# Performance work log

Hardware: AMD Instinct MI355X
Metric: run time of the kernel (lower is better)

The kernel has to match this reference:

```python
import jax, jax.numpy as jnp
import numpy as np

EPS = 1e-5

def _silu(x):
    return x * jax.nn.sigmoid(x)

def _layernorm(x, g, b):
    mu = jnp.mean(x, axis=-1, keepdims=True)
    var = jnp.mean((x - mu) ** 2, axis=-1, keepdims=True)
    return (x - mu) * jax.lax.rsqrt(var + EPS) * g + b

def _mamba(x, in_w, conv_w, conv_b, xproj_w, dt_w, dt_b, A_log, Dp, out_w):
    # x: (B, L, dm); faithful mamba-ssm block: in_proj -> causal dwconv -> silu ->
    # x_proj -> softplus(dt_proj) -> selective scan -> gate -> out_proj
    B, L, dm = x.shape
    di, K = conv_w.shape          # d_inner, d_conv
    ds = A_log.shape[1]           # d_state
    dtr = dt_w.shape[1]           # dt_rank
    xz = x @ in_w.T               # (B, L, 2*di)
    xi, z = jnp.split(xz, 2, axis=-1)
    # causal depthwise conv1d (pad K-1 on the left), kernel unrolled (K=4)
    xpad = jnp.pad(xi, ((0, 0), (K - 1, 0), (0, 0)))
    xc = conv_b + sum(conv_w[:, k] * xpad[:, k:k + L, :] for k in range(K))
    xc = _silu(xc)                # (B, L, di)
    xdbl = xc @ xproj_w.T         # (B, L, dtr + 2*ds)
    dt, Bm, Cm = jnp.split(xdbl, [dtr, dtr + ds], axis=-1)
    delta = jax.nn.softplus(dt @ dt_w.T + dt_b)        # (B, L, di)
    A = -jnp.exp(A_log)                                # (di, ds)
    dA = jnp.exp(delta[..., None] * A)                 # (B, L, di, ds)
    dBu = delta[..., None] * Bm[:, :, None, :] * xc[..., None]
    def step(h, inp):
        dA_t, dBu_t, C_t = inp                         # (B,di,ds),(B,di,ds),(B,ds)
        h = dA_t * h + dBu_t
        y = jnp.einsum('bdn,bn->bd', h, C_t)
        return h, y
    h0 = jnp.zeros((B, di, ds), dtype=x.dtype)
    _, ys = jax.lax.scan(step, h0, (dA.transpose(1, 0, 2, 3),
                                    dBu.transpose(1, 0, 2, 3),
                                    Cm.transpose(1, 0, 2)))
    y = ys.transpose(1, 0, 2) + xc * Dp                # (B, L, di)
    y = y * _silu(z)
    return y @ out_w.T                                 # (B, L, dm)

def _forward(t1, t2, t3, t4, t5,
             m0_in_w, m0_conv_w, m0_conv_b, m0_xproj_w, m0_dt_w, m0_dt_b, m0_Alog, m0_D, m0_out_w,
             m1_in_w, m1_conv_w, m1_conv_b, m1_xproj_w, m1_dt_w, m1_dt_b, m1_Alog, m1_D, m1_out_w,
             norm_g, norm_b, proj_w, proj_b, norm1_g, norm1_b, proj1_w, proj1_b, skip_scale):
    B = t1.shape[0]
    flat = lambda t, c: t.reshape(B, c, -1).transpose(0, 2, 1)   # (B, N, C)
    f1, f2, f3, f4, f5 = flat(t1, 8), flat(t2, 16), flat(t3, 24), flat(t4, 32), flat(t5, 48)
    c1 = jnp.concatenate([f1[:, :, 0:8], f2[:, :, 0:8], f3[:, :, 0:8], f4[:, :, 0:8], f5[:, :, 0:8]], axis=1)   # (B,21824,8)
    c2 = jnp.concatenate([f2[:, :, 8:16], f3[:, :, 8:16], f4[:, :, 8:16], f5[:, :, 8:16]], axis=1)              # (B,5440,8)
    c3 = jnp.concatenate([f3[:, :, 16:24], f4[:, :, 16:24], f5[:, :, 16:24]], axis=1)                           # (B,1344,8)
    c4 = jnp.concatenate([f4[:, :, 24:32], f5[:, :, 24:32]], axis=1)                                            # (B,320,8)
    c5 = f5[:, :, 32:48]                                                                                        # (B,64,16)
    def block8(c):
        y = _mamba(c, m0_in_w, m0_conv_w, m0_conv_b, m0_xproj_w, m0_dt_w, m0_dt_b, m0_Alog, m0_D, m0_out_w)
        return _layernorm(y + skip_scale * c, norm_g, norm_b) @ proj_w.T + proj_b
    x1m, x2m, x3m, x4m = block8(c1), block8(c2), block8(c3), block8(c4)
    y5 = _mamba(c5, m1_in_w, m1_conv_w, m1_conv_b, m1_xproj_w, m1_dt_w, m1_dt_b, m1_Alog, m1_D, m1_out_w)
    x5m = _layernorm(y5 + skip_scale * c5, norm1_g, norm1_b) @ proj1_w.T + proj1_b
    a1 = x1m[:, 0:16384, :]
    a2 = jnp.concatenate([x1m[:, 16384:20480, :], x2m[:, 0:4096, :]], axis=2)
    a3 = jnp.concatenate([x1m[:, 20480:21504, :], x2m[:, 4096:5120, :], x3m[:, 0:1024, :]], axis=2)
    a4 = jnp.concatenate([x1m[:, 21504:21760, :], x2m[:, 5120:5376, :], x3m[:, 1024:1280, :], x4m[:, 0:256, :]], axis=2)
    a5 = jnp.concatenate([x1m[:, 21760:, :], x2m[:, 5376:, :], x3m[:, 1280:, :], x4m[:, 256:, :], x5m], axis=2)
    x1 = a1.transpose(0, 2, 1).reshape(B, 8, 128, 128)
    x2 = a2.transpose(0, 2, 1).reshape(B, 16, 64, 64)
    x3 = a3.transpose(0, 2, 1).reshape(B, 24, 32, 32)
    x4 = a4.transpose(0, 2, 1).reshape(B, 32, 16, 16)
    x5 = a5.transpose(0, 2, 1).reshape(B, 48, 8, 8)
    return (x1, x2, x3, x4, x5)

def setup_inputs() -> dict:
    key = jax.random.key(0)
    ks = iter(jax.random.split(key, 64))
    B = 8
    def n(shape, s=1.0):
        return jax.random.normal(next(ks), shape, dtype=jnp.float32) * s
    inp = {
        't1': n((B, 8, 128, 128)), 't2': n((B, 16, 64, 64)), 't3': n((B, 24, 32, 32)),
        't4': n((B, 32, 16, 16)), 't5': n((B, 48, 8, 8)),
    }
    def mamba_params(pfx, dm):
        di, ds, K, dtr = 2 * dm, 16, 4, 1  # expand=2, d_state=16, d_conv=4, dt_rank=ceil(dm/16)=1
        return {
            pfx + '_in_w': n((2 * di, dm), dm ** -0.5),
            pfx + '_conv_w': n((di, K), 0.3),
            pfx + '_conv_b': n((di,), 0.1),
            pfx + '_xproj_w': n((dtr + 2 * ds, di), di ** -0.5),
            pfx + '_dt_w': n((di, dtr), 1.0),
            pfx + '_dt_b': n((di,), 0.1) - 3.0,
            pfx + '_Alog': jnp.log(jnp.tile(jnp.arange(1.0, ds + 1.0, dtype=jnp.float32), (di, 1))),
            pfx + '_D': jnp.ones((di,), jnp.float32),
            pfx + '_out_w': n((dm, di), di ** -0.5),
        }
    inp.update(mamba_params('m0', 8))
    inp.update(mamba_params('m1', 16))
    inp.update({
        'norm_g': jnp.ones((8,), jnp.float32), 'norm_b': jnp.zeros((8,), jnp.float32),
        'proj_w': n((8, 8), 8 ** -0.5), 'proj_b': jnp.zeros((8,), jnp.float32),
        'norm1_g': jnp.ones((16,), jnp.float32), 'norm1_b': jnp.zeros((16,), jnp.float32),
        'proj1_w': n((16, 16), 16 ** -0.5), 'proj1_b': jnp.zeros((16,), jnp.float32),
        'skip_scale': jnp.ones((1,), jnp.float32),
    })
    return inp

def reference(t1, t2, t3, t4, t5,
              m0_in_w, m0_conv_w, m0_conv_b, m0_xproj_w, m0_dt_w, m0_dt_b, m0_Alog, m0_D, m0_out_w,
              m1_in_w, m1_conv_w, m1_conv_b, m1_xproj_w, m1_dt_w, m1_dt_b, m1_Alog, m1_D, m1_out_w,
              norm_g, norm_b, proj_w, proj_b, norm1_g, norm1_b, proj1_w, proj1_b, skip_scale):
    return _forward(t1, t2, t3, t4, t5,
                    m0_in_w, m0_conv_w, m0_conv_b, m0_xproj_w, m0_dt_w, m0_dt_b, m0_Alog, m0_D, m0_out_w,
                    m1_in_w, m1_conv_w, m1_conv_b, m1_xproj_w, m1_dt_w, m1_dt_b, m1_Alog, m1_D, m1_out_w,
                    norm_g, norm_b, proj_w, proj_b, norm1_g, norm1_b, proj1_w, proj1_b, skip_scale)
```

## Files before the change

kernel.cpp:

```cpp
#include <hip/hip_runtime.h>
#include <cmath>

#define SCH 128
#define SUB 32
#define NCB 228
#define NCHUNK 1824
#define NSUB 7296
#define LOG2E 1.442695041f
#define LN2F  0.6931471806f
#define EXP2F(x) __builtin_exp2f(x)
#define LOG2F(x) __builtin_log2f(x)
#define SW_IN 0
#define SW_CONVW 256
#define SW_CONVB 320
#define SW_XPROJ 336
#define SW_DTW 864
#define SW_DTB 880
#define SW_A 896
#define SW_D 1152
#define SW_OUTW 1168
#define SW_NG 1296
#define SW_NB 1304
#define SW_PW 1312
#define SW_PB 1376
#define SW_SKIP 1384
#define REC 1392
#define RSTR 25
#define GR_C 3200
#define GR_X8 4224
#define GRECW 4736
#define SMEMP1 4592
#define C3 4592
#define X83 5616
#define YOF 6128
#define V_IN 0
#define V_CONVW 1024
#define V_CONVB 1152
#define V_XPROJ 1184
#define V_DTW 2240
#define V_DTB 2272
#define V_A 2304
#define V_D 2816
#define V_OUTW 2848
#define V_NG 3360
#define V_NB 3376
#define V_PW 3392
#define V_PB 3648
#define V_SKIP 3664
#define V_XC 3668
#define V_DL 5780
#define V_BM 7892
#define V_CM 8916
#define SMEM3 9940

struct Params {
  const float *t0, *t1, *t2, *t3, *t4;
  const float *in_w0,*conv_w0,*conv_b0,*xproj0,*dtw0,*dtb0,*Alog0,*D0,*outw0;
  const float *in_w1,*conv_w1,*conv_b1,*xproj1,*dtw1,*dtb1,*Alog1,*D1,*outw1;
  const float *ng,*nb,*pw,*pb,*n1g,*n1b,*p1w,*p1b,*skip;
  float* out;
  float *hloc, *sumdelta, *grec;
};

__device__ __forceinline__ float softplusf(float x) {
  float t = EXP2F(-fabsf(x) * LOG2E);
  return fmaxf(x, 0.f) + LOG2F(1.f + t) * LN2F;
}
__device__ __forceinline__ float siluf(float x) { return x * (1.f / (1.f + __expf(-x))); }
__device__ __forceinline__ unsigned pk(float a, float b) {
  unsigned ua = __float_as_uint(a) + 0x8000u;
  unsigned ub = __float_as_uint(b) + 0x8000u;
  return (ua >> 16) | (ub & 0xFFFF0000u);
}
__device__ __forceinline__ float lo16(unsigned w) { return __uint_as_float(w << 16); }
__device__ __forceinline__ float hi16(unsigned w) { return __uint_as_float(w & 0xFFFF0000u); }

struct Loc { int k, pos, ch, hw, C; };

__device__ __forceinline__ Loc locate(int seq, int l) {
  Loc r;
  if (seq == 0) { r.ch = 0;
    if (l < 16384)      { r.k=0; r.pos=l;        r.hw=16384; r.C=8;  }
    else if (l < 20480) { r.k=1; r.pos=l-16384;  r.hw=4096;  r.C=16; }
    else if (l < 21504) { r.k=2; r.pos=l-20480;  r.hw=1024;  r.C=24; }
    else if (l < 21760) { r.k=3; r.pos=l-21504;  r.hw=256;   r.C=32; }
    else                { r.k=4; r.pos=l-21760;  r.hw=64;    r.C=48; }
  } else if (seq == 1) { r.ch = 8;
    if (l < 4096)       { r.k=1; r.pos=l;        r.hw=4096;  r.C=16; }
    else if (l < 5120)  { r.k=2; r.pos=l-4096;   r.hw=1024;  r.C=24; }
    else if (l < 5376)  { r.k=3; r.pos=l-5120;   r.hw=256;   r.C=32; }
    else                { r.k=4; r.pos=l-5376;   r.hw=64;    r.C=48; }
  } else if (seq == 2) { r.ch = 16;
    if (l < 1024)       { r.k=2; r.pos=l;        r.hw=1024;  r.C=24; }
    else if (l < 1280)  { r.k=3; r.pos=l-1024;   r.hw=256;   r.C=32; }
    else                { r.k=4; r.pos=l-1280;   r.hw=64;    r.C=48; }
  } else { r.ch = 24;
    if (l < 256)        { r.k=3; r.pos=l;        r.hw=256;   r.C=32; }
    else                { r.k=4; r.pos=l-256;    r.hw=64;    r.C=48; }
  }
  return r;
}

__device__ __forceinline__ const float* tsel(const Params& p, int k) {
  switch (k) { case 0: return p.t0; case 1: return p.t1; case 2: return p.t2;
               case 3: return p.t3; default: return p.t4; }
}
__device__ __forceinline__ int outbase(int k) {
  switch (k) { case 0: return 0; case 1: return 1048576; case 2: return 1572864;
               case 3: return 1769472; default: return 1835008; }
}

__device__ __forceinline__ void gather8(const Params& p, int b, int seq, int l, float* c) {
  Loc lc = locate(seq, l);
  const float* t = tsel(p, lc.k);
  int base = (b * lc.C + lc.ch) * lc.hw + lc.pos;
  #pragma unroll
  for (int j = 0; j < 8; ++j) c[j] = t[base + j * lc.hw];
}

__device__ __forceinline__ void decode_bid(int bid, int& b, int& seq, int& l0, int& Sa) {
  b = bid / NCB;
  int r = bid - b * NCB;
  int c, L;
  if (r < 171)      { seq = 0; c = r;       L = 21824; }
  else if (r < 214) { seq = 1; c = r - 171; L = 5440;  }
  else if (r < 225) { seq = 2; c = r - 214; L = 1344;  }
  else              { seq = 3; c = r - 225; L = 320;   }
  l0 = c * SCH;
  int rem = L - l0;
  Sa = rem < SCH ? rem : SCH;
}

__device__ void load_w0(const Params& p, float* s, int tid) {
  for (int i = tid; i < 256; i += 256) s[SW_IN + i] = p.in_w0[i];
  for (int i = tid; i < 64;  i += 256) s[SW_CONVW + i] = p.conv_w0[i];
  for (int i = tid; i < 16;  i += 256) s[SW_CONVB + i] = p.conv_b0[i];
  for (int i = tid; i < 528; i += 256) s[SW_XPROJ + i] = p.xproj0[i];
  for (int i = tid; i < 16;  i += 256) s[SW_DTW + i] = p.dtw0[i];
  for (int i = tid; i < 16;  i += 256) s[SW_DTB + i] = p.dtb0[i];
  for (int i = tid; i < 256; i += 256) s[SW_A + i] = -__expf(p.Alog0[i]) * LOG2E;
  for (int i = tid; i < 16;  i += 256) s[SW_D + i] = p.D0[i];
  for (int i = tid; i < 128; i += 256) s[SW_OUTW + i] = p.outw0[i];
  for (int i = tid; i < 8;   i += 256) s[SW_NG + i] = p.ng[i];
  for (int i = tid; i < 8;   i += 256) s[SW_NB + i] = p.nb[i];
  for (int i = tid; i < 64;  i += 256) s[SW_PW + i] = p.pw[i];
  for (int i = tid; i < 8;   i += 256) s[SW_PB + i] = p.pb[i];
  if (tid == 0) s[SW_SKIP] = p.skip[0];
}

__device__ __forceinline__ float dot16h(const float* w, int ch0, int cho,
                                        const float* a, const float* o) {
  float4 wa0 = *(const float4*)&w[ch0];
  float4 wa1 = *(const float4*)&w[ch0 + 4];
  float4 wb0 = *(const float4*)&w[cho];
  float4 wb1 = *(const float4*)&w[cho + 4];
  float r = wa0.x * a[0];
  r = fmaf(wa0.y, a[1], r); r = fmaf(wa0.z, a[2], r); r = fmaf(wa0.w, a[3], r);
  r = fmaf(wa1.x, a[4], r); r = fmaf(wa1.y, a[5], r);
  r = fmaf(wa1.z, a[6], r); r = fmaf(wa1.w, a[7], r);
  r = fmaf(wb0.x, o[0], r); r = fmaf(wb0.y, o[1], r);
  r = fmaf(wb0.z, o[2], r); r = fmaf(wb0.w, o[3], r);
  r = fmaf(wb1.x, o[4], r); r = fmaf(wb1.y, o[5], r);
  r = fmaf(wb1.z, o[6], r); r = fmaf(wb1.w, o[7], r);
  return r;
}

__global__ __launch_bounds__(256, 8) void k_pass1(Params p) {
  __shared__ float s[SMEMP1];
  int tid = threadIdx.x;
  int cid = blockIdx.x;
  int b, seq, l0, Sa;
  decode_bid(cid, b, seq, l0, Sa);
  int tok = tid >> 1, hf = tid & 1;
  int ch0 = hf * 8, cho = 8 - ch0;
  bool act = tok < Sa;
  bool grow = tok < Sa + 3;
  bool hrow = (Sa == SCH) && (tok >= SCH - 3);
  unsigned* gc = (unsigned*)(p.grec + (size_t)cid * GRECW);
  float x8[8], x8h[8];
  {
    int l = l0 - 3 + tok;
    if (grow && l >= 0) gather8(p, b, seq, l, x8);
    else {
      #pragma unroll
      for (int j = 0; j < 8; ++j) x8[j] = 0.f;
    }
  }
  if (hrow) gather8(p, b, seq, l0 + tok, x8h);
  load_w0(p, s, tid);
  if (hf == 0) {
    if (grow && tok >= 3) {
      uint4 v = make_uint4(pk(x8[0], x8[1]), pk(x8[2], x8[3]),
                           pk(x8[4], x8[5]), pk(x8[6], x8[7]));
      *(uint4*)&gc[GR_X8 + (tok - 3) * 4] = v;
    }
    if (hrow) {
      uint4 v = make_uint4(pk(x8h[0], x8h[1]), pk(x8h[2], x8h[3]),
                           pk(x8h[4], x8h[5]), pk(x8h[6], x8h[7]));
      *(uint4*)&gc[GR_X8 + tok * 4] = v;
    }
  }
  __syncthreads();
  if (grow) {
    #pragma unroll
    for (int ii = 0; ii < 8; ++ii) {
      int i = ch0 + ii;
      float4 wa = *(const float4*)&s[SW_IN + i * 8];
      float4 wb = *(const float4*)&s[SW_IN + i * 8 + 4];
      float a = wa.x * x8[0];
      a = fmaf(wa.y, x8[1], a); a = fmaf(wa.z, x8[2], a); a = fmaf(wa.w, x8[3], a);
      a = fmaf(wb.x, x8[4], a); a = fmaf(wb.y, x8[5], a);
      a = fmaf(wb.z, x8[6], a); a = fmaf(wb.w, x8[7], a);
      s[REC + tok * 17 + i] = a;
    }
  }
  if (hrow) {
    int r = tok + 3;
    #pragma unroll
    for (int ii = 0; ii < 8; ++ii) {
      int i = ch0 + ii;
      float4 wa = *(const float4*)&s[SW_IN + i * 8];
      float4 wb = *(const float4*)&s[SW_IN + i * 8 + 4];
      float a = wa.x * x8h[0];
      a = fmaf(wa.y, x8h[1], a); a = fmaf(wa.z, x8h[2], a); a = fmaf(wa.w, x8h[3], a);
      a = fmaf(wb.x, x8h[4], a); a = fmaf(wb.y, x8h[5], a);
      a = fmaf(wb.z, x8h[6], a); a = fmaf(wb.w, x8h[7], a);
      s[REC + r * 17 + i] = a;
    }
  }
  __syncthreads();
  float xc8[8], xco[8];
  float dt = 0.f;
  if (act) {
    #pragma unroll
    for (int ii = 0; ii < 8; ++ii) {
      int i = ch0 + ii;
      float4 cw = *(const float4*)&s[SW_CONVW + i * 4];
      float a = s[SW_CONVB + i];
      a = fmaf(cw.x, s[REC + (tok + 0) * 17 + i], a);
      a = fmaf(cw.y, s[REC + (tok + 1) * 17 + i], a);
      a = fmaf(cw.z, s[REC + (tok + 2) * 17 + i], a);
      a = fmaf(cw.w, s[REC + (tok + 3) * 17 + i], a);
      xc8[ii] = siluf(a);
    }
    #pragma unroll
    for (int ii = 0; ii < 8; ++ii) xco[ii] = __shfl_xor(xc8[ii], 1);
    dt = dot16h(&s[SW_XPROJ], ch0, cho, xc8, xco);
  }
  __syncthreads();
  unsigned* ru = (unsigned*)&s[REC + tok * RSTR];
  if (act) {
    #pragma unroll
    for (int q = 0; q < 4; ++q) {
      int d0 = ch0 + 2 * q;
      float da = softplusf(fmaf(dt, s[SW_DTW + d0],     s[SW_DTB + d0]));
      float db = softplusf(fmaf(dt, s[SW_DTW + d0 + 1], s[SW_DTB + d0 + 1]));
      ru[hf * 4 + q]     = pk(da, db);
      ru[8 + hf * 4 + q] = pk(xc8[2*q], xc8[2*q + 1]);
    }
    #pragma unroll
    for (int q = 0; q < 4; ++q) {
      int n0 = ch0 + 2 * q;
      float a0 = dot16h(&s[SW_XPROJ + (1 + n0) * 16], ch0, cho, xc8, xco);
      float a1 = dot16h(&s[SW_XPROJ + (2 + n0) * 16], ch0, cho, xc8, xco);
      ru[16 + hf * 4 + q] = pk(a0, a1);
    }
    uint4 cv;
    {
      int n0 = ch0;
      float a0 = dot16h(&s[SW_XPROJ + (17 + n0) * 16], ch0, cho, xc8, xco);
      float a1 = dot16h(&s[SW_XPROJ + (18 + n0) * 16], ch0, cho, xc8, xco);
      float a2 = dot16h(&s[SW_XPROJ + (19 + n0) * 16], ch0, cho, xc8, xco);
      float a3 = dot16h(&s[SW_XPROJ + (20 + n0) * 16], ch0, cho, xc8, xco);
      float a4 = dot16h(&s[SW_XPROJ + (21 + n0) * 16], ch0, cho, xc8, xco);
      float a5 = dot16h(&s[SW_XPROJ + (22 + n0) * 16], ch0, cho, xc8, xco);
      float a6 = dot16h(&s[SW_XPROJ + (23 + n0) * 16], ch0, cho, xc8, xco);
      float a7 = dot16h(&s[SW_XPROJ + (24 + n0) * 16], ch0, cho, xc8, xco);
      cv = make_uint4(pk(a0, a1), pk(a2, a3), pk(a4, a5), pk(a6, a7));
    }
    *(uint4*)&gc[GR_C + tok * 8 + hf * 4] = cv;
  } else {
    #pragma unroll
    for (int q = 0; q < 4; ++q) {
      ru[hf * 4 + q] = 0u;
      ru[8 + hf * 4 + q] = 0u;
      ru[16 + hf * 4 + q] = 0u;
    }
    *(uint4*)&gc[GR_C + tok * 8 + hf * 4] = make_uint4(0u, 0u, 0u, 0u);
  }
  __syncthreads();
  const unsigned* su = (const unsigned*)s;
  {
    uint4* g4 = (uint4*)gc;
    const uint4* s4 = (const uint4*)&su[REC];
    #pragma unroll 2
    for (int i4 = tid; i4 < GR_C / 4; i4 += 256) g4[i4] = s4[i4];
  }
  int w = tid >> 6, lane = tid & 63;
  int d = lane >> 2, ng = lane & 3;
  int dh = d >> 1;
  bool dodd = d & 1;
  int t0 = w * SUB;
  float4 Av = *(float4*)&s[SW_A + d * 16 + ng * 4];
  float h0 = 0.f, h1 = 0.f, h2 = 0.f, h3 = 0.f, sd = 0.f;
  for (int tile = 0; tile < 8; ++tile) {
    int tb = t0 + tile * 4;
    unsigned wd[4], wx[4]; uint2 wB[4];
    #pragma unroll
    for (int i = 0; i < 4; ++i) {
      int base = REC + (tb + i) * RSTR;
      wd[i] = su[base + dh];
      wx[i] = su[base + 8 + dh];
      wB[i] = *(const uint2*)&su[base + 16 + ng * 2];
    }
    #pragma unroll
    for (int i = 0; i < 4; ++i) {
      float dl = dodd ? hi16(wd[i]) : lo16(wd[i]);
      float u = dl * (dodd ? hi16(wx[i]) : lo16(wx[i]));
      float e0 = EXP2F(Av.x * dl), e1 = EXP2F(Av.y * dl);
      float e2 = EXP2F(Av.z * dl), e3 = EXP2F(Av.w * dl);
      h0 = fmaf(e0, h0, u * lo16(wB[i].x));
      h1 = fmaf(e1, h1, u * hi16(wB[i].x));
      h2 = fmaf(e2, h2, u * lo16(wB[i].y));
      h3 = fmaf(e3, h3, u * hi16(wB[i].y));
      sd += dl;
    }
  }
  int gs = cid * 4 + w;
  unsigned* hu = (unsigned*)p.hloc;
  hu[gs * 128 + d * 8 + ng * 2]     = pk(h0, h1);
  hu[gs * 128 + d * 8 + ng * 2 + 1] = pk(h2, h3);
  if (ng == 0) p.sumdelta[(size_t)gs * 16 + d] = sd;
}

__device__ void load_w1(const Params& p, float* s, int tid) {
  for (int i = tid; i < 1024; i += 256) s[V_IN + i] = p.in_w1[i];
  for (int i = tid; i < 128;  i += 256) s[V_CONVW + i] = p.conv_w1[i];
  for (int i = tid; i < 32;   i += 256) s[V_CONVB + i] = p.conv_b1[i];
  for (int i = tid; i < 1056; i += 256) s[V_XPROJ + i] = p.xproj1[i];
  for (int i = tid; i < 32;   i += 256) s[V_DTW + i] = p.dtw1[i];
  for (int i = tid; i < 32;   i += 256) s[V_DTB + i] = p.dtb1[i];
  for (int i = tid; i < 512;  i += 256) s[V_A + i] = -__expf(p.Alog1[i]) * LOG2E;
  for (int i = tid; i < 32;   i += 256) s[V_D + i] = p.D1[i];
  for (int i = tid; i < 512;  i += 256) s[V_OUTW + i] = p.outw1[i];
  for (int i = tid; i < 16;   i += 256) s[V_NG + i] = p.n1g[i];
  for (int i = tid; i < 16;   i += 256) s[V_NB + i] = p.n1b[i];
  for (int i = tid; i < 256;  i += 256) s[V_PW + i] = p.p1w[i];
  for (int i = tid; i < 16;   i += 256) s[V_PB + i] = p.p1b[i];
  if (tid == 0) s[V_SKIP] = p.skip[0];
}

__device__ void c5_path(const Params& p, float* s, int b, int tid) {
  load_w1(p, s, tid);
  int og = tid >> 6, tok = tid & 63;
  float x16[16];
  #pragma unroll
  for (int j = 0; j < 16; ++j) x16[j] = p.t4[(b * 48 + 32 + j) * 64 + tok];
  __syncthreads();
  #pragma unroll
  for (int ii = 0; ii < 8; ++ii) {
    int i = og * 8 + ii;
    float a = 0.f;
    #pragma unroll
    for (int j = 0; j < 16; ++j) a = fmaf(s[V_IN + i * 16 + j], x16[j], a);
    float xm1 = __shfl_up(a, 1);
    float xm2 = __shfl_up(a, 2);
    float xm3 = __shfl_up(a, 3);
    float c = s[V_CONVB + i];
    c = fmaf(s[V_CONVW + i * 4 + 3], a, c);
    if (tok >= 1) c = fmaf(s[V_CONVW + i * 4 + 2], xm1, c);
    if (tok >= 2) c = fmaf(s[V_CONVW + i * 4 + 1], xm2, c);
    if (tok >= 3) c = fmaf(s[V_CONVW + i * 4 + 0], xm3, c);
    s[V_XC + tok * 33 + i] = siluf(c);
  }
  __syncthreads();
  float xcr[32];
  #pragma unroll
  for (int i = 0; i < 32; ++i) xcr[i] = s[V_XC + tok * 33 + i];
  float dt = 0.f;
  #pragma unroll
  for (int i = 0; i < 32; ++i) dt = fmaf(s[V_XPROJ + i], xcr[i], dt);
  #pragma unroll
  for (int nn = 0; nn < 4; ++nn) {
    int n = og * 4 + nn;
    float aB = 0.f, aC = 0.f;
    #pragma unroll
    for (int i = 0; i < 32; ++i) {
      aB = fmaf(s[V_XPROJ + (1 + n) * 32 + i], xcr[i], aB);
      aC = fmaf(s[V_XPROJ + (17 + n) * 32 + i], xcr[i], aC);
    }
    s[V_BM + tok * 16 + n] = aB;
    s[V_CM + tok * 16 + n] = aC;
  }
  #pragma unroll
  for (int ii = 0; ii < 8; ++ii) {
    int d = og * 8 + ii;
    s[V_DL + tok * 33 + d] = softplusf(fmaf(dt, s[V_DTW + d], s[V_DTB + d]));
  }
  __syncthreads();
  if (tid < 128) {
    int d = tid >> 2, ng = tid & 3;
    float4 Av = *(float4*)&s[V_A + d * 16 + ng * 4];
    float h0 = 0.f, h1 = 0.f, h2 = 0.f, h3 = 0.f;
    for (int tile = 0; tile < 16; ++tile) {
      int tb = tile * 4;
      float dl[4], xv[4]; float4 bm[4], cm[4];
      #pragma unroll
      for (int i = 0; i < 4; ++i) {
        dl[i] = s[V_DL + (tb + i) * 33 + d];
        xv[i] = s[V_XC + (tb + i) * 33 + d];
        bm[i] = *(float4*)&s[V_BM + (tb + i) * 16 + ng * 4];
        cm[i] = *(float4*)&s[V_CM + (tb + i) * 16 + ng * 4];
      }
      float yp[4];
      #pragma unroll
      for (int i = 0; i < 4; ++i) {
        float u = dl[i] * xv[i];
        float e0 = EXP2F(Av.x * dl[i]), e1 = EXP2F(Av.y * dl[i]);
        float e2 = EXP2F(Av.z * dl[i]), e3 = EXP2F(Av.w * dl[i]);
        h0 = fmaf(e0, h0, u * bm[i].x);
        h1 = fmaf(e1, h1, u * bm[i].y);
        h2 = fmaf(e2, h2, u * bm[i].z);
        h3 = fmaf(e3, h3, u * bm[i].w);
        float y = h0 * cm[i].x;
        y = fmaf(h1, cm[i].y, y); y = fmaf(h2, cm[i].z, y); y = fmaf(h3, cm[i].w, y);
        yp[i] = y;
      }
      #pragma unroll
      for (int i = 0; i < 4; ++i) yp[i] += __shfl_xor(yp[i], 1);
      #pragma unroll
      for (int i = 0; i < 4; ++i) yp[i] += __shfl_xor(yp[i], 2);
      float ysel = ng == 0 ? yp[0] : ng == 1 ? yp[1] : ng == 2 ? yp[2] : yp[3];
      s[V_DL + (tb + ng) * 33 + d] = ysel;
    }
  }
  __syncthreads();
  #pragma unroll
  for (int ii = 0; ii < 8; ++ii) {
    int d = og * 8 + ii;
    float z = 0.f;
    #pragma unroll
    for (int j = 0; j < 16; ++j) z = fmaf(s[V_IN + (32 + d) * 16 + j], x16[j], z);
    float yv = (s[V_DL + tok * 33 + d] + s[V_XC + tok * 33 + d] * s[V_D + d]) * siluf(z);
    s[V_DL + tok * 33 + d] = yv;
  }
  __syncthreads();
  float yr[32];
  #pragma unroll
  for (int d = 0; d < 32; ++d) yr[d] = s[V_DL + tok * 33 + d];
  float sk = s[V_SKIP];
  #pragma unroll
  for (int mm = 0; mm < 4; ++mm) {
    int m = og * 4 + mm;
    float a = sk * x16[m];
    #pragma unroll
    for (int d = 0; d < 32; ++d) a = fmaf(s[V_OUTW + m * 32 + d], yr[d], a);
    s[V_XC + tok * 33 + m] = a;
  }
  __syncthreads();
  if (tid < 64) {
    float ov[16];
    #pragma unroll
    for (int m = 0; m < 16; ++m) ov[m] = s[V_XC + tok * 33 + m];
    float mu = 0.f;
    #pragma unroll
    for (int m = 0; m < 16; ++m) mu += ov[m];
    mu *= (1.f / 16.f);
    float var = 0.f;
    #pragma unroll
    for (int m = 0; m < 16; ++m) { float t = ov[m] - mu; var += t * t; }
    var *= (1.f / 16.f);
    float inv = rsqrtf(var + 1e-5f);
    #pragma unroll
    for (int m = 0; m < 16; ++m)
      s[V_XC + tok * 33 + m] = (ov[m] - mu) * inv * s[V_NG + m] + s[V_NB + m];
  }
  __syncthreads();
  float lr[16];
  #pragma unroll
  for (int j = 0; j < 16; ++j) lr[j] = s[V_XC + tok * 33 + j];
  #pragma unroll
  for (int mm = 0; mm < 4; ++mm) {
    int m = og * 4 + mm;
    float a = s[V_PB + m];
    #pragma unroll
    for (int j = 0; j < 16; ++j) a = fmaf(s[V_PW + m * 16 + j], lr[j], a);
    p.out[1835008 + (b * 48 + 32 + m) * 64 + tok] = a;
  }
}

__global__ __launch_bounds__(256) void k_pass2(Params p) {
  __shared__ unsigned sh[684 * 8];
  __shared__ float ssd[684];
  __shared__ float sS[32];
  __shared__ float sH[512];
  int bid = blockIdx.x, tid = threadIdx.x;
  int b = bid >> 6;
  int rr = bid & 63;
  int seq = rr >> 4, d = rr & 15;
  const int nch[4] = {171, 43, 11, 3};
  const int chf[4] = {0, 171, 214, 225};
  int nsub = nch[seq] * 4;
  int g0 = (b * NCB + chf[seq]) * 4;
  unsigned* hu = (unsigned*)p.hloc;
  int n8 = nsub * 8;
  for (int wdx = tid; wdx < n8; wdx += 256) {
    int rec = wdx >> 3, pr_ = wdx & 7;
    sh[wdx] = hu[(size_t)(g0 + rec) * 128 + d * 8 + pr_];
  }
  for (int rec = tid; rec < nsub; rec += 256)
    ssd[rec] = p.sumdelta[(size_t)(g0 + rec) * 16 + d];
  int g = tid >> 3, pr = tid & 7;
  float A0 = -__expf(p.Alog0[d * 16 + pr * 2]) * LOG2E;
  float A1 = -__expf(p.Alog0[d * 16 + pr * 2 + 1]) * LOG2E;
  __syncthreads();
  int T = (nsub + 31) >> 5;
  int i0 = g * T;
  int i1 = i0 + T; if (i1 > nsub) i1 = nsub;
  float S = 0.f, h0 = 0.f, h1 = 0.f;
  for (int i = i0; i < i1; ++i) {
    unsigned wl = sh[i * 8 + pr];
    float sv = ssd[i];
    float e0 = EXP2F(A0 * sv), e1 = EXP2F(A1 * sv);
    h0 = fmaf(e0, h0, lo16(wl));
    h1 = fmaf(e1, h1, hi16(wl));
    S += sv;
  }
  if (pr == 0) sS[g] = S;
  sH[g * 16 + pr * 2]     = h0;
  sH[g * 16 + pr * 2 + 1] = h1;
  __syncthreads();
  float q0 = 0.f, q1 = 0.f;
  for (int j = 0; j < g; ++j) {
    float Sj = sS[j];
    float e0 = EXP2F(A0 * Sj), e1 = EXP2F(A1 * Sj);
    q0 = fmaf(e0, q0, sH[j * 16 + pr * 2]);
    q1 = fmaf(e1, q1, sH[j * 16 + pr * 2 + 1]);
  }
  for (int i = i0; i < i1; ++i) {
    unsigned wl = sh[i * 8 + pr];
    float sv = ssd[i];
    sh[i * 8 + pr] = pk(q0, q1);
    float e0 = EXP2F(A0 * sv), e1 = EXP2F(A1 * sv);
    q0 = fmaf(e0, q0, lo16(wl));
    q1 = fmaf(e1, q1, hi16(wl));
  }
  __syncthreads();
  for (int wdx = tid; wdx < n8; wdx += 256) {
    int rec = wdx >> 3, pr_ = wdx & 7;
    hu[(size_t)(g0 + rec) * 128 + d * 8 + pr_] = sh[wdx];
  }
}

__global__ __launch_bounds__(256, 4) void k_pass3(Params p) {
  __shared__ float s[SMEM3];
  int tid = threadIdx.x;
  if (blockIdx.x < 8) { c5_path(p, s, blockIdx.x, tid); return; }
  load_w0(p, s, tid);
  int w = tid >> 6, lane = tid & 63;
  int d = lane >> 2, ng = lane & 3;
  int dh = d >> 1;
  bool dodd = d & 1;
  int t0 = w * SUB;
  int tok = tid >> 1, hf = tid & 1, ch0 = hf * 8;
  const unsigned* su = (const unsigned*)s;
  int cid = blockIdx.x - 8;
  int b, seq, l0, Sa;
  decode_bid(cid, b, seq, l0, Sa);
  {
    const uint4* g4 = (const uint4*)(p.grec + (size_t)cid * GRECW);
    uint4* s4 = (uint4*)&((unsigned*)s)[REC];
    #pragma unroll 2
    for (int i4 = tid; i4 < GRECW / 4; i4 += 256) s4[i4] = g4[i4];
  }
  __syncthreads();
  int gs = cid * 4 + w;
  float4 Av = *(float4*)&s[SW_A + d * 16 + ng * 4];
  const unsigned* hu = (const unsigned*)p.hloc;
  unsigned hw0 = hu[gs * 128 + d * 8 + ng * 2];
  unsigned hw1 = hu[gs * 128 + d * 8 + ng * 2 + 1];
  float h0 = lo16(hw0), h1 = hi16(hw0), h2 = lo16(hw1), h3 = hi16(hw1);
  for (int tile = 0; tile < 8; ++tile) {
    int tb = t0 + tile * 4;
    unsigned wd[4], wx[4]; uint2 wB[4], wC[4];
    #pragma unroll
    for (int i = 0; i < 4; ++i) {
      int base = REC + (tb + i) * RSTR;
      wd[i] = su[base + dh];
      wx[i] = su[base + 8 + dh];
      wB[i] = *(const uint2*)&su[base + 16 + ng * 2];
      wC[i] = *(const uint2*)&su[C3 + (tb + i) * 8 + ng * 2];
    }
    float yp[4];
    #pragma unroll
    for (int i = 0; i < 4; ++i) {
      float dl = dodd ? hi16(wd[i]) : lo16(wd[i]);
      float u = dl * (dodd ? hi16(wx[i]) : lo16(wx[i]));
      float e0 = EXP2F(Av.x * dl), e1 = EXP2F(Av.y * dl);
      float e2 = EXP2F(Av.z * dl), e3 = EXP2F(Av.w * dl);
      h0 = fmaf(e0, h0, u * lo16(wB[i].x));
      h1 = fmaf(e1, h1, u * hi16(wB[i].x));
      h2 = fmaf(e2, h2, u * lo16(wB[i].y));
      h3 = fmaf(e3, h3, u * hi16(wB[i].y));
      float y = h0 * lo16(wC[i].x);
      y = fmaf(h1, hi16(wC[i].x), y);
      y = fmaf(h2, lo16(wC[i].y), y);
      y = fmaf(h3, hi16(wC[i].y), y);
      yp[i] = y;
    }
    #pragma unroll
    for (int i = 0; i < 4; ++i) yp[i] += __shfl_xor(yp[i], 1);
    #pragma unroll
    for (int i = 0; i < 4; ++i) yp[i] += __shfl_xor(yp[i], 2);
    float ysel = ng == 0 ? yp[0] : ng == 1 ? yp[1] : ng == 2 ? yp[2] : yp[3];
    s[YOF + (tb + ng) * 17 + d] = ysel;
  }
  __syncthreads();
  if (tok < Sa) {
    const unsigned* xp = (const unsigned*)&s[X83 + tok * 4];
    float c8[8];
    #pragma unroll
    for (int q = 0; q < 4; ++q) { c8[2*q] = lo16(xp[q]); c8[2*q+1] = hi16(xp[q]); }
    const unsigned* ru = (const unsigned*)&s[REC + tok * RSTR];
    float yv8[8];
    #pragma unroll
    for (int q = 0; q < 4; ++q) {
      unsigned wv = ru[8 + hf * 4 + q];
      int d0 = ch0 + 2 * q;
      float4 w0a = *(const float4*)&s[SW_IN + (16 + d0) * 8];
      float4 w0b = *(const float4*)&s[SW_IN + (16 + d0) * 8 + 4];
      float4 w1a = *(const float4*)&s[SW_IN + (17 + d0) * 8];
      float4 w1b = *(const float4*)&s[SW_IN + (17 + d0) * 8 + 4];
      float z0 = w0a.x * c8[0];
      z0 = fmaf(w0a.y, c8[1], z0); z0 = fmaf(w0a.z, c8[2], z0); z0 = fmaf(w0a.w, c8[3], z0);
      z0 = fmaf(w0b.x, c8[4], z0); z0 = fmaf(w0b.y, c8[5], z0);
      z0 = fmaf(w0b.z, c8[6], z0); z0 = fmaf(w0b.w, c8[7], z0);
      float z1 = w1a.x * c8[0];
      z1 = fmaf(w1a.y, c8[1], z1); z1 = fmaf(w1a.z, c8[2], z1); z1 = fmaf(w1a.w, c8[3], z1);
      z1 = fmaf(w1b.x, c8[4], z1); z1 = fmaf(w1b.y, c8[5], z1);
      z1 = fmaf(w1b.z, c8[6], z1); z1 = fmaf(w1b.w, c8[7], z1);
      yv8[2*q]   = (s[YOF + tok * 17 + d0]     + lo16(wv) * s[SW_D + d0])     * siluf(z0);
      yv8[2*q+1] = (s[YOF + tok * 17 + d0 + 1] + hi16(wv) * s[SW_D + d0 + 1]) * siluf(z1);
    }
    float o[8];
    float sk = s[SW_SKIP];
    #pragma unroll
    for (int m = 0; m < 8; ++m) {
      float4 wv0 = *(const float4*)&s[SW_OUTW + m * 16 + ch0];
      float4 wv1 = *(const float4*)&s[SW_OUTW + m * 16 + ch0 + 4];
      float a = wv0.x * yv8[0];
      a = fmaf(wv0.y, yv8[1], a); a = fmaf(wv0.z, yv8[2], a); a = fmaf(wv0.w, yv8[3], a);
      a = fmaf(wv1.x, yv8[4], a); a = fmaf(wv1.y, yv8[5], a);
      a = fmaf(wv1.z, yv8[6], a); a = fmaf(wv1.w, yv8[7], a);
      a += __shfl_xor(a, 1);
      o[m] = a + sk * c8[m];
    }
    float mu = 0.f;
    #pragma unroll
    for (int m = 0; m < 8; ++m) mu += o[m];
    mu *= 0.125f;
    float var = 0.f;
    #pragma unroll
    for (int m = 0; m < 8; ++m) { float t = o[m] - mu; var += t * t; }
    var *= 0.125f;
    float inv = rsqrtf(var + 1e-5f);
    #pragma unroll
    for (int m = 0; m < 8; ++m) o[m] = (o[m] - mu) * inv * s[SW_NG + m] + s[SW_NB + m];
    Loc lc = locate(seq, l0 + tok);
    int obase = outbase(lc.k) + (b * lc.C + lc.ch) * lc.hw + lc.pos;
    #pragma unroll
    for (int mm = 0; mm < 4; ++mm) {
      int m = hf * 4 + mm;
      float4 pw0 = *(const float4*)&s[SW_PW + m * 8];
      float4 pw1 = *(const float4*)&s[SW_PW + m * 8 + 4];
      float a = s[SW_PB + m];
      a = fmaf(pw0.x, o[0], a); a = fmaf(pw0.y, o[1], a);
      a = fmaf(pw0.z, o[2], a); a = fmaf(pw0.w, o[3], a);
      a = fmaf(pw1.x, o[4], a); a = fmaf(pw1.y, o[5], a);
      a = fmaf(pw1.z, o[6], a); a = fmaf(pw1.w, o[7], a);
      p.out[obase + m * lc.hw] = a;
    }
  }
}

extern "C" void kernel_launch(void* const* d_in, const int* in_sizes, int n_in,
                              void* d_out, int out_size, void* d_ws, size_t ws_size,
                              hipStream_t stream) {
  (void)in_sizes; (void)n_in; (void)out_size; (void)ws_size;
  Params p;
  p.t0 = (const float*)d_in[0];  p.t1 = (const float*)d_in[1];
  p.t2 = (const float*)d_in[2];  p.t3 = (const float*)d_in[3];
  p.t4 = (const float*)d_in[4];
  p.in_w0   = (const float*)d_in[5];
  p.conv_w0 = (const float*)d_in[6];
  p.conv_b0 = (const float*)d_in[7];
  p.xproj0  = (const float*)d_in[8];
  p.dtw0    = (const float*)d_in[9];
  p.dtb0    = (const float*)d_in[10];
  p.Alog0   = (const float*)d_in[11];
  p.D0      = (const float*)d_in[12];
  p.outw0   = (const float*)d_in[13];
  p.in_w1   = (const float*)d_in[14];
  p.conv_w1 = (const float*)d_in[15];
  p.conv_b1 = (const float*)d_in[16];
  p.xproj1  = (const float*)d_in[17];
  p.dtw1    = (const float*)d_in[18];
  p.dtb1    = (const float*)d_in[19];
  p.Alog1   = (const float*)d_in[20];
  p.D1      = (const float*)d_in[21];
  p.outw1   = (const float*)d_in[22];
  p.ng  = (const float*)d_in[23];
  p.nb  = (const float*)d_in[24];
  p.pw  = (const float*)d_in[25];
  p.pb  = (const float*)d_in[26];
  p.n1g = (const float*)d_in[27];
  p.n1b = (const float*)d_in[28];
  p.p1w = (const float*)d_in[29];
  p.p1b = (const float*)d_in[30];
  p.skip = (const float*)d_in[31];
  p.out = (float*)d_out;
  float* ws = (float*)d_ws;
  p.hloc     = ws;
  p.sumdelta = ws + (size_t)NSUB * 128;
  p.grec     = ws + (size_t)NSUB * 128 + (size_t)NSUB * 16;
  k_pass1<<<dim3(NCHUNK), dim3(256), 0, stream>>>(p);
  k_pass2<<<dim3(512), dim3(256), 0, stream>>>(p);
  k_pass3<<<dim3(NCHUNK + 8), dim3(256), 0, stream>>>(p);
}
```

Measured before the change: 113.9 us.

## Fuse three-pass chunked scan into one kernel with decoupled look-back flags

Replaces the three launches (local chunk scan, cross-chunk prefix scan, recompute and output) with a single fused kernel. Each block computes its chunk aggregate, publishes it through global flags and an aggregate buffer, then spin-waits on earlier chunks and folds their states serially before the final scan. This removes the global round-trip of per-chunk records and the launch overhead of two extra kernels. The cost is a serial look-back over every earlier chunk, spin-waiting that relies on earlier blocks being scheduled first, and an added memset. The C5 path also reads some weights directly from global memory and stores B and C as packed bf16.

```diff
diff --git a/kernel.cpp b/kernel.cpp
--- a/kernel.cpp
+++ b/kernel.cpp
@@ -5,7 +5,6 @@
 #define SUB 32
 #define NCB 228
 #define NCHUNK 1824
-#define NSUB 7296
 #define LOG2E 1.442695041f
 #define LN2F  0.6931471806f
 #define EXP2F(x) __builtin_exp2f(x)
@@ -24,34 +23,28 @@
 #define SW_PW 1312
 #define SW_PB 1376
 #define SW_SKIP 1384
+#define SCRH 256
+#define SCRS 768
 #define REC 1392
 #define RSTR 25
-#define GR_C 3200
-#define GR_X8 4224
-#define GRECW 4736
-#define SMEMP1 4592
-#define C3 4592
-#define X83 5616
-#define YOF 6128
-#define V_IN 0
-#define V_CONVW 1024
-#define V_CONVB 1152
-#define V_XPROJ 1184
-#define V_DTW 2240
-#define V_DTB 2272
-#define V_A 2304
-#define V_D 2816
-#define V_OUTW 2848
-#define V_NG 3360
-#define V_NB 3376
-#define V_PW 3392
-#define V_PB 3648
-#define V_SKIP 3664
-#define V_XC 3668
-#define V_DL 5780
-#define V_BM 7892
-#define V_CM 8916
-#define SMEM3 9940
+#define C3f 4592
+#define X83f 5616
+#define SMEMF 6272
+#define AGGW 160
+#define W_CONVW 0
+#define W_CONVB 128
+#define W_DTW 160
+#define W_DTB 192
+#define W_A 224
+#define W_D 736
+#define W_NG 768
+#define W_NB 784
+#define W_PB 800
+#define W_SKIP 816
+#define W_XC 820
+#define W_DL 2932
+#define W_BM 5044
+#define W_CM 5556
 
 struct Params {
   const float *t0, *t1, *t2, *t3, *t4;
@@ -59,7 +52,8 @@
   const float *in_w1,*conv_w1,*conv_b1,*xproj1,*dtw1,*dtb1,*Alog1,*D1,*outw1;
   const float *ng,*nb,*pw,*pb,*n1g,*n1b,*p1w,*p1b,*skip;
   float* out;
-  float *hloc, *sumdelta, *grec;
+  unsigned* flags;
+  float* agg;
 };
 
 __device__ __forceinline__ float softplusf(float x) {
@@ -165,192 +159,21 @@
   return r;
 }
 
-__global__ __launch_bounds__(256, 8) void k_pass1(Params p) {
-  __shared__ float s[SMEMP1];
-  int tid = threadIdx.x;
-  int cid = blockIdx.x;
-  int b, seq, l0, Sa;
-  decode_bid(cid, b, seq, l0, Sa);
-  int tok = tid >> 1, hf = tid & 1;
-  int ch0 = hf * 8, cho = 8 - ch0;
-  bool act = tok < Sa;
-  bool grow = tok < Sa + 3;
-  bool hrow = (Sa == SCH) && (tok >= SCH - 3);
-  unsigned* gc = (unsigned*)(p.grec + (size_t)cid * GRECW);
-  float x8[8], x8h[8];
-  {
-    int l = l0 - 3 + tok;
-    if (grow && l >= 0) gather8(p, b, seq, l, x8);
-    else {
-      #pragma unroll
-      for (int j = 0; j < 8; ++j) x8[j] = 0.f;
-    }
-  }
-  if (hrow) gather8(p, b, seq, l0 + tok, x8h);
-  load_w0(p, s, tid);
-  if (hf == 0) {
-    if (grow && tok >= 3) {
-      uint4 v = make_uint4(pk(x8[0], x8[1]), pk(x8[2], x8[3]),
-                           pk(x8[4], x8[5]), pk(x8[6], x8[7]));
-      *(uint4*)&gc[GR_X8 + (tok - 3) * 4] = v;
-    }
-    if (hrow) {
-      uint4 v = make_uint4(pk(x8h[0], x8h[1]), pk(x8h[2], x8h[3]),
-                           pk(x8h[4], x8h[5]), pk(x8h[6], x8h[7]));
-      *(uint4*)&gc[GR_X8 + tok * 4] = v;
-    }
-  }
-  __syncthreads();
-  if (grow) {
-    #pragma unroll
-    for (int ii = 0; ii < 8; ++ii) {
-      int i = ch0 + ii;
-      float4 wa = *(const float4*)&s[SW_IN + i * 8];
-      float4 wb = *(const float4*)&s[SW_IN + i * 8 + 4];
-      float a = wa.x * x8[0];
-      a = fmaf(wa.y, x8[1], a); a = fmaf(wa.z, x8[2], a); a = fmaf(wa.w, x8[3], a);
-      a = fmaf(wb.x, x8[4], a); a = fmaf(wb.y, x8[5], a);
-      a = fmaf(wb.z, x8[6], a); a = fmaf(wb.w, x8[7], a);
-      s[REC + tok * 17 + i] = a;
-    }
-  }
-  if (hrow) {
-    int r = tok + 3;
-    #pragma unroll
-    for (int ii = 0; ii < 8; ++ii) {
-      int i = ch0 + ii;
-      float4 wa = *(const float4*)&s[SW_IN + i * 8];
-      float4 wb = *(const float4*)&s[SW_IN + i * 8 + 4];
-      float a = wa.x * x8h[0];
-      a = fmaf(wa.y, x8h[1], a); a = fmaf(wa.z, x8h[2], a); a = fmaf(wa.w, x8h[3], a);
-      a = fmaf(wb.x, x8h[4], a); a = fmaf(wb.y, x8h[5], a);
-      a = fmaf(wb.z, x8h[6], a); a = fmaf(wb.w, x8h[7], a);
-      s[REC + r * 17 + i] = a;
-    }
-  }
-  __syncthreads();
-  float xc8[8], xco[8];
-  float dt = 0.f;
-  if (act) {
-    #pragma unroll
-    for (int ii = 0; ii < 8; ++ii) {
-      int i = ch0 + ii;
-      float4 cw = *(const float4*)&s[SW_CONVW + i * 4];
-      float a = s[SW_CONVB + i];
-      a = fmaf(cw.x, s[REC + (tok + 0) * 17 + i], a);
-      a = fmaf(cw.y, s[REC + (tok + 1) * 17 + i], a);
-      a = fmaf(cw.z, s[REC + (tok + 2) * 17 + i], a);
-      a = fmaf(cw.w, s[REC + (tok + 3) * 17 + i], a);
-      xc8[ii] = siluf(a);
-    }
-    #pragma unroll
-    for (int ii = 0; ii < 8; ++ii) xco[ii] = __shfl_xor(xc8[ii], 1);
-    dt = dot16h(&s[SW_XPROJ], ch0, cho, xc8, xco);
-  }
-  __syncthreads();
-  unsigned* ru = (unsigned*)&s[REC + tok * RSTR];
-  if (act) {
-    #pragma unroll
-    for (int q = 0; q < 4; ++q) {
-      int d0 = ch0 + 2 * q;
-      float da = softplusf(fmaf(dt, s[SW_DTW + d0],     s[SW_DTB + d0]));
-      float db = softplusf(fmaf(dt, s[SW_DTW + d0 + 1], s[SW_DTB + d0 + 1]));
-      ru[hf * 4 + q]     = pk(da, db);
-      ru[8 + hf * 4 + q] = pk(xc8[2*q], xc8[2*q + 1]);
-    }
-    #pragma unroll
-    for (int q = 0; q < 4; ++q) {
-      int n0 = ch0 + 2 * q;
-      float a0 = dot16h(&s[SW_XPROJ + (1 + n0) * 16], ch0, cho, xc8, xco);
-      float a1 = dot16h(&s[SW_XPROJ + (2 + n0) * 16], ch0, cho, xc8, xco);
-      ru[16 + hf * 4 + q] = pk(a0, a1);
-    }
-    uint4 cv;
-    {
-      int n0 = ch0;
-      float a0 = dot16h(&s[SW_XPROJ + (17 + n0) * 16], ch0, cho, xc8, xco);
-      float a1 = dot16h(&s[SW_XPROJ + (18 + n0) * 16], ch0, cho, xc8, xco);
-      float a2 = dot16h(&s[SW_XPROJ + (19 + n0) * 16], ch0, cho, xc8, xco);
-      float a3 = dot16h(&s[SW_XPROJ + (20 + n0) * 16], ch0, cho, xc8, xco);
-      float a4 = dot16h(&s[SW_XPROJ + (21 + n0) * 16], ch0, cho, xc8, xco);
-      float a5 = dot16h(&s[SW_XPROJ + (22 + n0) * 16], ch0, cho, xc8, xco);
-      float a6 = dot16h(&s[SW_XPROJ + (23 + n0) * 16], ch0, cho, xc8, xco);
-      float a7 = dot16h(&s[SW_XPROJ + (24 + n0) * 16], ch0, cho, xc8, xco);
-      cv = make_uint4(pk(a0, a1), pk(a2, a3), pk(a4, a5), pk(a6, a7));
-    }
-    *(uint4*)&gc[GR_C + tok * 8 + hf * 4] = cv;
-  } else {
-    #pragma unroll
-    for (int q = 0; q < 4; ++q) {
-      ru[hf * 4 + q] = 0u;
-      ru[8 + hf * 4 + q] = 0u;
-      ru[16 + hf * 4 + q] = 0u;
-    }
-    *(uint4*)&gc[GR_C + tok * 8 + hf * 4] = make_uint4(0u, 0u, 0u, 0u);
-  }
-  __syncthreads();
-  const unsigned* su = (const unsigned*)s;
-  {
-    uint4* g4 = (uint4*)gc;
-    const uint4* s4 = (const uint4*)&su[REC];
-    #pragma unroll 2
-    for (int i4 = tid; i4 < GR_C / 4; i4 += 256) g4[i4] = s4[i4];
-  }
-  int w = tid >> 6, lane = tid & 63;
-  int d = lane >> 2, ng = lane & 3;
-  int dh = d >> 1;
-  bool dodd = d & 1;
-  int t0 = w * SUB;
-  float4 Av = *(float4*)&s[SW_A + d * 16 + ng * 4];
-  float h0 = 0.f, h1 = 0.f, h2 = 0.f, h3 = 0.f, sd = 0.f;
-  for (int tile = 0; tile < 8; ++tile) {
-    int tb = t0 + tile * 4;
-    unsigned wd[4], wx[4]; uint2 wB[4];
-    #pragma unroll
-    for (int i = 0; i < 4; ++i) {
-      int base = REC + (tb + i) * RSTR;
-      wd[i] = su[base + dh];
-      wx[i] = su[base + 8 + dh];
-      wB[i] = *(const uint2*)&su[base + 16 + ng * 2];
-    }
-    #pragma unroll
-    for (int i = 0; i < 4; ++i) {
-      float dl = dodd ? hi16(wd[i]) : lo16(wd[i]);
-      float u = dl * (dodd ? hi16(wx[i]) : lo16(wx[i]));
-      float e0 = EXP2F(Av.x * dl), e1 = EXP2F(Av.y * dl);
-      float e2 = EXP2F(Av.z * dl), e3 = EXP2F(Av.w * dl);
-      h0 = fmaf(e0, h0, u * lo16(wB[i].x));
-      h1 = fmaf(e1, h1, u * hi16(wB[i].x));
-      h2 = fmaf(e2, h2, u * lo16(wB[i].y));
-      h3 = fmaf(e3, h3, u * hi16(wB[i].y));
-      sd += dl;
-    }
-  }
-  int gs = cid * 4 + w;
-  unsigned* hu = (unsigned*)p.hloc;
-  hu[gs * 128 + d * 8 + ng * 2]     = pk(h0, h1);
-  hu[gs * 128 + d * 8 + ng * 2 + 1] = pk(h2, h3);
-  if (ng == 0) p.sumdelta[(size_t)gs * 16 + d] = sd;
-}
-
 __device__ void load_w1(const Params& p, float* s, int tid) {
-  for (int i = tid; i < 1024; i += 256) s[V_IN + i] = p.in_w1[i];
-  for (int i = tid; i < 128;  i += 256) s[V_CONVW + i] = p.conv_w1[i];
-  for (int i = tid; i < 32;   i += 256) s[V_CONVB + i] = p.conv_b1[i];
-  for (int i = tid; i < 1056; i += 256) s[V_XPROJ + i] = p.xproj1[i];
-  for (int i = tid; i < 32;   i += 256) s[V_DTW + i] = p.dtw1[i];
-  for (int i = tid; i < 32;   i += 256) s[V_DTB + i] = p.dtb1[i];
-  for (int i = tid; i < 512;  i += 256) s[V_A + i] = -__expf(p.Alog1[i]) * LOG2E;
-  for (int i = tid; i < 32;   i += 256) s[V_D + i] = p.D1[i];
-  for (int i = tid; i < 512;  i += 256) s[V_OUTW + i] = p.outw1[i];
-  for (int i = tid; i < 16;   i += 256) s[V_NG + i] = p.n1g[i];
-  for (int i = tid; i < 16;   i += 256) s[V_NB + i] = p.n1b[i];
-  for (int i = tid; i < 256;  i += 256) s[V_PW + i] = p.p1w[i];
-  for (int i = tid; i < 16;   i += 256) s[V_PB + i] = p.p1b[i];
-  if (tid == 0) s[V_SKIP] = p.skip[0];
+  for (int i = tid; i < 128; i += 256) s[W_CONVW + i] = p.conv_w1[i];
+  for (int i = tid; i < 32;  i += 256) s[W_CONVB + i] = p.conv_b1[i];
+  for (int i = tid; i < 32;  i += 256) s[W_DTW + i] = p.dtw1[i];
+  for (int i = tid; i < 32;  i += 256) s[W_DTB + i] = p.dtb1[i];
+  for (int i = tid; i < 512; i += 256) s[W_A + i] = -__expf(p.Alog1[i]) * LOG2E;
+  for (int i = tid; i < 32;  i += 256) s[W_D + i] = p.D1[i];
+  for (int i = tid; i < 16;  i += 256) s[W_NG + i] = p.n1g[i];
+  for (int i = tid; i < 16;  i += 256) s[W_NB + i] = p.n1b[i];
+  for (int i = tid; i < 16;  i += 256) s[W_PB + i] = p.p1b[i];
+  if (tid == 0) s[W_SKIP] = p.skip[0];
 }
 
 __device__ void c5_path(const Params& p, float* s, int b, int tid) {
+  unsigned* su32 = (unsigned*)s;
   load_w1(p, s, tid);
   int og = tid >> 6, tok = tid & 63;
   float x16[16];
@@ -362,55 +185,61 @@
     int i = og * 8 + ii;
     float a = 0.f;
     #pragma unroll
-    for (int j = 0; j < 16; ++j) a = fmaf(s[V_IN + i * 16 + j], x16[j], a);
+    for (int j = 0; j < 16; ++j) a = fmaf(p.in_w1[i * 16 + j], x16[j], a);
     float xm1 = __shfl_up(a, 1);
     float xm2 = __shfl_up(a, 2);
     float xm3 = __shfl_up(a, 3);
-    float c = s[V_CONVB + i];
-    c = fmaf(s[V_CONVW + i * 4 + 3], a, c);
-    if (tok >= 1) c = fmaf(s[V_CONVW + i * 4 + 2], xm1, c);
-    if (tok >= 2) c = fmaf(s[V_CONVW + i * 4 + 1], xm2, c);
-    if (tok >= 3) c = fmaf(s[V_CONVW + i * 4 + 0], xm3, c);
-    s[V_XC + tok * 33 + i] = siluf(c);
+    float c = s[W_CONVB + i];
+    c = fmaf(s[W_CONVW + i * 4 + 3], a, c);
+    if (tok >= 1) c = fmaf(s[W_CONVW + i * 4 + 2], xm1, c);
+    if (tok >= 2) c = fmaf(s[W_CONVW + i * 4 + 1], xm2, c);
+    if (tok >= 3) c = fmaf(s[W_CONVW + i * 4 + 0], xm3, c);
+    s[W_XC + tok * 33 + i] = siluf(c);
   }
   __syncthreads();
   float xcr[32];
   #pragma unroll
-  for (int i = 0; i < 32; ++i) xcr[i] = s[V_XC + tok * 33 + i];
+  for (int i = 0; i < 32; ++i) xcr[i] = s[W_XC + tok * 33 + i];
   float dt = 0.f;
   #pragma unroll
-  for (int i = 0; i < 32; ++i) dt = fmaf(s[V_XPROJ + i], xcr[i], dt);
+  for (int i = 0; i < 32; ++i) dt = fmaf(p.xproj1[i], xcr[i], dt);
+  float aB[4], aC[4];
   #pragma unroll
   for (int nn = 0; nn < 4; ++nn) {
     int n = og * 4 + nn;
-    float aB = 0.f, aC = 0.f;
+    float vB = 0.f, vC = 0.f;
     #pragma unroll
     for (int i = 0; i < 32; ++i) {
-      aB = fmaf(s[V_XPROJ + (1 + n) * 32 + i], xcr[i], aB);
-      aC = fmaf(s[V_XPROJ + (17 + n) * 32 + i], xcr[i], aC);
-    }
-    s[V_BM + tok * 16 + n] = aB;
-    s[V_CM + tok * 16 + n] = aC;
-  }
+      vB = fmaf(p.xproj1[(1 + n) * 32 + i], xcr[i], vB);
+      vC = fmaf(p.xproj1[(17 + n) * 32 + i], xcr[i], vC);
+    }
+    aB[nn] = vB; aC[nn] = vC;
+  }
+  su32[W_BM + tok * 8 + og * 2]     = pk(aB[0], aB[1]);
+  su32[W_BM + tok * 8 + og * 2 + 1] = pk(aB[2], aB[3]);
+  su32[W_CM + tok * 8 + og * 2]     = pk(aC[0], aC[1]);
+  su32[W_CM + tok * 8 + og * 2 + 1] = pk(aC[2], aC[3]);
   #pragma unroll
   for (int ii = 0; ii < 8; ++ii) {
     int d = og * 8 + ii;
-    s[V_DL + tok * 33 + d] = softplusf(fmaf(dt, s[V_DTW + d], s[V_DTB + d]));
+    s[W_DL + tok * 33 + d] = softplusf(fmaf(dt, s[W_DTW + d], s[W_DTB + d]));
   }
   __syncthreads();
   if (tid < 128) {
     int d = tid >> 2, ng = tid & 3;
-    float4 Av = *(float4*)&s[V_A + d * 16 + ng * 4];
+    float4 Av = *(float4*)&s[W_A + d * 16 + ng * 4];
     float h0 = 0.f, h1 = 0.f, h2 = 0.f, h3 = 0.f;
     for (int tile = 0; tile < 16; ++tile) {
       int tb = tile * 4;
       float dl[4], xv[4]; float4 bm[4], cm[4];
       #pragma unroll
       for (int i = 0; i < 4; ++i) {
-        dl[i] = s[V_DL + (tb + i) * 33 + d];
-        xv[i] = s[V_XC + (tb + i) * 33 + d];
-        bm[i] = *(float4*)&s[V_BM + (tb + i) * 16 + ng * 4];
-        cm[i] = *(float4*)&s[V_CM + (tb + i) * 16 + ng * 4];
+        dl[i] = s[W_DL + (tb + i) * 33 + d];
+        xv[i] = s[W_XC + (tb + i) * 33 + d];
+        uint2 bw = *(const uint2*)&su32[W_BM + (tb + i) * 8 + ng * 2];
+        uint2 cw = *(const uint2*)&su32[W_CM + (tb + i) * 8 + ng * 2];
+        bm[i] = make_float4(lo16(bw.x), hi16(bw.x), lo16(bw.y), hi16(bw.y));
+        cm[i] = make_float4(lo16(cw.x), hi16(cw.x), lo16(cw.y), hi16(cw.y));
       }
       float yp[4];
       #pragma unroll
@@ -431,7 +260,7 @@
       #pragma unroll
       for (int i = 0; i < 4; ++i) yp[i] += __shfl_xor(yp[i], 2);
       float ysel = ng == 0 ? yp[0] : ng == 1 ? yp[1] : ng == 2 ? yp[2] : yp[3];
-      s[V_DL + (tb + ng) * 33 + d] = ysel;
+      s[W_DL + (tb + ng) * 33 + d] = ysel;
     }
   }
   __syncthreads();
@@ -440,28 +269,28 @@
     int d = og * 8 + ii;
     float z = 0.f;
     #pragma unroll
-    for (int j = 0; j < 16; ++j) z = fmaf(s[V_IN + (32 + d) * 16 + j], x16[j], z);
-    float yv = (s[V_DL + tok * 33 + d] + s[V_XC + tok * 33 + d] * s[V_D + d]) * siluf(z);
-    s[V_DL + tok * 33 + d] = yv;
+    for (int j = 0; j < 16; ++j) z = fmaf(p.in_w1[(32 + d) * 16 + j], x16[j], z);
+    float yv = (s[W_DL + tok * 33 + d] + s[W_XC + tok * 33 + d] * s[W_D + d]) * siluf(z);
+    s[W_DL + tok * 33 + d] = yv;
   }
   __syncthreads();
   float yr[32];
   #pragma unroll
-  for (int d = 0; d < 32; ++d) yr[d] = s[V_DL + tok * 33 + d];
-  float sk = s[V_SKIP];
+  for (int d = 0; d < 32; ++d) yr[d] = s[W_DL + tok * 33 + d];
+  float sk = s[W_SKIP];
   #pragma unroll
   for (int mm = 0; mm < 4; ++mm) {
     int m = og * 4 + mm;
     float a = sk * x16[m];
     #pragma unroll
-    for (int d = 0; d < 32; ++d) a = fmaf(s[V_OUTW + m * 32 + d], yr[d], a);
-    s[V_XC + tok * 33 + m] = a;
+    for (int d = 0; d < 32; ++d) a = fmaf(p.outw1[m * 32 + d], yr[d], a);
+    s[W_XC + tok * 33 + m] = a;
   }
   __syncthreads();
   if (tid < 64) {
     float ov[16];
     #pragma unroll
-    for (int m = 0; m < 16; ++m) ov[m] = s[V_XC + tok * 33 + m];
+    for (int m = 0; m < 16; ++m) ov[m] = s[W_XC + tok * 33 + m];
     float mu = 0.f;
     #pragma unroll
     for (int m = 0; m < 16; ++m) mu += ov[m];
@@ -473,159 +302,289 @@
     float inv = rsqrtf(var + 1e-5f);
     #pragma unroll
     for (int m = 0; m < 16; ++m)
-      s[V_XC + tok * 33 + m] = (ov[m] - mu) * inv * s[V_NG + m] + s[V_NB + m];
+      s[W_XC + tok * 33 + m] = (ov[m] - mu) * inv * s[W_NG + m] + s[W_NB + m];
   }
   __syncthreads();
   float lr[16];
   #pragma unroll
-  for (int j = 0; j < 16; ++j) lr[j] = s[V_XC + tok * 33 + j];
+  for (int j = 0; j < 16; ++j) lr[j] = s[W_XC + tok * 33 + j];
   #pragma unroll
   for (int mm = 0; mm < 4; ++mm) {
     int m = og * 4 + mm;
-    float a = s[V_PB + m];
-    #pragma unroll
-    for (int j = 0; j < 16; ++j) a = fmaf(s[V_PW + m * 16 + j], lr[j], a);
+    float a = s[W_PB + m];
+    #pragma unroll
+    for (int j = 0; j < 16; ++j) a = fmaf(p.p1w[m * 16 + j], lr[j], a);
     p.out[1835008 + (b * 48 + 32 + m) * 64 + tok] = a;
   }
 }
 
-__global__ __launch_bounds__(256) void k_pass2(Params p) {
-  __shared__ unsigned sh[684 * 8];
-  __shared__ float ssd[684];
-  __shared__ float sS[32];
-  __shared__ float sH[512];
-  int bid = blockIdx.x, tid = threadIdx.x;
-  int b = bid >> 6;
-  int rr = bid & 63;
-  int seq = rr >> 4, d = rr & 15;
-  const int nch[4] = {171, 43, 11, 3};
-  const int chf[4] = {0, 171, 214, 225};
-  int nsub = nch[seq] * 4;
-  int g0 = (b * NCB + chf[seq]) * 4;
-  unsigned* hu = (unsigned*)p.hloc;
-  int n8 = nsub * 8;
-  for (int wdx = tid; wdx < n8; wdx += 256) {
-    int rec = wdx >> 3, pr_ = wdx & 7;
-    sh[wdx] = hu[(size_t)(g0 + rec) * 128 + d * 8 + pr_];
-  }
-  for (int rec = tid; rec < nsub; rec += 256)
-    ssd[rec] = p.sumdelta[(size_t)(g0 + rec) * 16 + d];
-  int g = tid >> 3, pr = tid & 7;
-  float A0 = -__expf(p.Alog0[d * 16 + pr * 2]) * LOG2E;
-  float A1 = -__expf(p.Alog0[d * 16 + pr * 2 + 1]) * LOG2E;
-  __syncthreads();
-  int T = (nsub + 31) >> 5;
-  int i0 = g * T;
-  int i1 = i0 + T; if (i1 > nsub) i1 = nsub;
-  float S = 0.f, h0 = 0.f, h1 = 0.f;
-  for (int i = i0; i < i1; ++i) {
-    unsigned wl = sh[i * 8 + pr];
-    float sv = ssd[i];
-    float e0 = EXP2F(A0 * sv), e1 = EXP2F(A1 * sv);
-    h0 = fmaf(e0, h0, lo16(wl));
-    h1 = fmaf(e1, h1, hi16(wl));
-    S += sv;
-  }
-  if (pr == 0) sS[g] = S;
-  sH[g * 16 + pr * 2]     = h0;
-  sH[g * 16 + pr * 2 + 1] = h1;
-  __syncthreads();
-  float q0 = 0.f, q1 = 0.f;
-  for (int j = 0; j < g; ++j) {
-    float Sj = sS[j];
-    float e0 = EXP2F(A0 * Sj), e1 = EXP2F(A1 * Sj);
-    q0 = fmaf(e0, q0, sH[j * 16 + pr * 2]);
-    q1 = fmaf(e1, q1, sH[j * 16 + pr * 2 + 1]);
-  }
-  for (int i = i0; i < i1; ++i) {
-    unsigned wl = sh[i * 8 + pr];
-    float sv = ssd[i];
-    sh[i * 8 + pr] = pk(q0, q1);
-    float e0 = EXP2F(A0 * sv), e1 = EXP2F(A1 * sv);
-    q0 = fmaf(e0, q0, lo16(wl));
-    q1 = fmaf(e1, q1, hi16(wl));
-  }
-  __syncthreads();
-  for (int wdx = tid; wdx < n8; wdx += 256) {
-    int rec = wdx >> 3, pr_ = wdx & 7;
-    hu[(size_t)(g0 + rec) * 128 + d * 8 + pr_] = sh[wdx];
-  }
-}
-
-__global__ __launch_bounds__(256, 4) void k_pass3(Params p) {
-  __shared__ float s[SMEM3];
+__global__ __launch_bounds__(256, 6) void k_fused(Params p) {
+  __shared__ float s[SMEMF];
+  unsigned* su32 = (unsigned*)s;
   int tid = threadIdx.x;
   if (blockIdx.x < 8) { c5_path(p, s, blockIdx.x, tid); return; }
+  int cid = blockIdx.x - 8;
+  int b, seq, l0, Sa;
+  decode_bid(cid, b, seq, l0, Sa);
+  const int chf_[4] = {0, 171, 214, 225};
+  int c0 = b * NCB + chf_[seq];
+  int tok = tid >> 1, hf = tid & 1;
+  int ch0 = hf * 8, cho = 8 - ch0;
+  bool act = tok < Sa;
+  bool grow = tok < Sa + 3;
+  bool hrow = (Sa == SCH) && (tok >= SCH - 3);
+  float x8[8], x8h[8];
+  {
+    int l = l0 - 3 + tok;
+    if (grow && l >= 0) gather8(p, b, seq, l, x8);
+    else {
+      #pragma unroll
+      for (int j = 0; j < 8; ++j) x8[j] = 0.f;
+    }
+  }
+  if (hrow) gather8(p, b, seq, l0 + tok, x8h);
   load_w0(p, s, tid);
+  if (hf == 0) {
+    if (grow && tok >= 3) {
+      uint4 v = make_uint4(pk(x8[0], x8[1]), pk(x8[2], x8[3]),
+                           pk(x8[4], x8[5]), pk(x8[6], x8[7]));
+      *(uint4*)&su32[X83f + (tok - 3) * 4] = v;
+    }
+    if (hrow) {
+      uint4 v = make_uint4(pk(x8h[0], x8h[1]), pk(x8h[2], x8h[3]),
+                           pk(x8h[4], x8h[5]), pk(x8h[6], x8h[7]));
+      *(uint4*)&su32[X83f + tok * 4] = v;
+    }
+  }
+  __syncthreads();
+  if (grow) {
+    #pragma unroll
+    for (int ii = 0; ii < 8; ++ii) {
+      int i = ch0 + ii;
+      float4 wa = *(const float4*)&s[SW_IN + i * 8];
+      float4 wb = *(const float4*)&s[SW_IN + i * 8 + 4];
+      float a = wa.x * x8[0];
+      a = fmaf(wa.y, x8[1], a); a = fmaf(wa.z, x8[2], a); a = fmaf(wa.w, x8[3], a);
+      a = fmaf(wb.x, x8[4], a); a = fmaf(wb.y, x8[5], a);
+      a = fmaf(wb.z, x8[6], a); a = fmaf(wb.w, x8[7], a);
+      s[REC + tok * 17 + i] = a;
+    }
+  }
+  if (hrow) {
+    int r = tok + 3;
+    #pragma unroll
+    for (int ii = 0; ii < 8; ++ii) {
+      int i = ch0 + ii;
+      float4 wa = *(const float4*)&s[SW_IN + i * 8];
+      float4 wb = *(const float4*)&s[SW_IN + i * 8 + 4];
+      float a = wa.x * x8h[0];
+      a = fmaf(wa.y, x8h[1], a); a = fmaf(wa.z, x8h[2], a); a = fmaf(wa.w, x8h[3], a);
+      a = fmaf(wb.x, x8h[4], a); a = fmaf(wb.y, x8h[5], a);
+      a = fmaf(wb.z, x8h[6], a); a = fmaf(wb.w, x8h[7], a);
+      s[REC + r * 17 + i] = a;
+    }
+  }
+  __syncthreads();
+  float xc8[8], xco[8];
+  float dt = 0.f;
+  if (act) {
+    #pragma unroll
+    for (int ii = 0; ii < 8; ++ii) {
+      int i = ch0 + ii;
+      float4 cw = *(const float4*)&s[SW_CONVW + i * 4];
+      float a = s[SW_CONVB + i];
+      a = fmaf(cw.x, s[REC + (tok + 0) * 17 + i], a);
+      a = fmaf(cw.y, s[REC + (tok + 1) * 17 + i], a);
+      a = fmaf(cw.z, s[REC + (tok + 2) * 17 + i], a);
+      a = fmaf(cw.w, s[REC + (tok + 3) * 17 + i], a);
+      xc8[ii] = siluf(a);
+    }
+    #pragma unroll
+    for (int ii = 0; ii < 8; ++ii) xco[ii] = __shfl_xor(xc8[ii], 1);
+    dt = dot16h(&s[SW_XPROJ], ch0, cho, xc8, xco);
+  }
+  __syncthreads();
+  unsigned* ru = &su32[REC + tok * RSTR];
+  if (act) {
+    #pragma unroll
+    for (int q = 0; q < 4; ++q) {
+      int d0 = ch0 + 2 * q;
+      float da = softplusf(fmaf(dt, s[SW_DTW + d0],     s[SW_DTB + d0]));
+      float db = softplusf(fmaf(dt, s[SW_DTW + d0 + 1], s[SW_DTB + d0 + 1]));
+      ru[hf * 4 + q]     = pk(da, db);
+      ru[8 + hf * 4 + q] = pk(xc8[2*q], xc8[2*q + 1]);
+    }
+    #pragma unroll
+    for (int q = 0; q < 4; ++q) {
+      int n0 = ch0 + 2 * q;
+      float a0 = dot16h(&s[SW_XPROJ + (1 + n0) * 16], ch0, cho, xc8, xco);
+      float a1 = dot16h(&s[SW_XPROJ + (2 + n0) * 16], ch0, cho, xc8, xco);
+      ru[16 + hf * 4 + q] = pk(a0, a1);
+    }
+    uint4 cv;
+    {
+      float a0 = dot16h(&s[SW_XPROJ + (17 + ch0) * 16], ch0, cho, xc8, xco);
+      float a1 = dot16h(&s[SW_XPROJ + (18 + ch0) * 16], ch0, cho, xc8, xco);
+      float a2 = dot16h(&s[SW_XPROJ + (19 + ch0) * 16], ch0, cho, xc8, xco);
+      float a3 = dot16h(&s[SW_XPROJ + (20 + ch0) * 16], ch0, cho, xc8, xco);
+      float a4 = dot16h(&s[SW_XPROJ + (21 + ch0) * 16], ch0, cho, xc8, xco);
+      float a5 = dot16h(&s[SW_XPROJ + (22 + ch0) * 16], ch0, cho, xc8, xco);
+      float a6 = dot16h(&s[SW_XPROJ + (23 + ch0) * 16], ch0, cho, xc8, xco);
+      float a7 = dot16h(&s[SW_XPROJ + (24 + ch0) * 16], ch0, cho, xc8, xco);
+      cv = make_uint4(pk(a0, a1), pk(a2, a3), pk(a4, a5), pk(a6, a7));
+    }
+    *(uint4*)&su32[C3f + tok * 8 + hf * 4] = cv;
+  } else {
+    #pragma unroll
+    for (int q = 0; q < 4; ++q) {
+      ru[hf * 4 + q] = 0u;
+      ru[8 + hf * 4 + q] = 0u;
+      ru[16 + hf * 4 + q] = 0u;
+    }
+    *(uint4*)&su32[C3f + tok * 8 + hf * 4] = make_uint4(0u, 0u, 0u, 0u);
+  }
+  __syncthreads();
   int w = tid >> 6, lane = tid & 63;
   int d = lane >> 2, ng = lane & 3;
   int dh = d >> 1;
   bool dodd = d & 1;
   int t0 = w * SUB;
-  int tok = tid >> 1, hf = tid & 1, ch0 = hf * 8;
-  const unsigned* su = (const unsigned*)s;
-  int cid = blockIdx.x - 8;
-  int b, seq, l0, Sa;
-  decode_bid(cid, b, seq, l0, Sa);
   {
-    const uint4* g4 = (const uint4*)(p.grec + (size_t)cid * GRECW);
-    uint4* s4 = (uint4*)&((unsigned*)s)[REC];
-    #pragma unroll 2
-    for (int i4 = tid; i4 < GRECW / 4; i4 += 256) s4[i4] = g4[i4];
-  }
-  __syncthreads();
-  int gs = cid * 4 + w;
-  float4 Av = *(float4*)&s[SW_A + d * 16 + ng * 4];
-  const unsigned* hu = (const unsigned*)p.hloc;
-  unsigned hw0 = hu[gs * 128 + d * 8 + ng * 2];
-  unsigned hw1 = hu[gs * 128 + d * 8 + ng * 2 + 1];
-  float h0 = lo16(hw0), h1 = hi16(hw0), h2 = lo16(hw1), h3 = hi16(hw1);
-  for (int tile = 0; tile < 8; ++tile) {
-    int tb = t0 + tile * 4;
-    unsigned wd[4], wx[4]; uint2 wB[4], wC[4];
-    #pragma unroll
-    for (int i = 0; i < 4; ++i) {
-      int base = REC + (tb + i) * RSTR;
-      wd[i] = su[base + dh];
-      wx[i] = su[base + 8 + dh];
-      wB[i] = *(const uint2*)&su[base + 16 + ng * 2];
-      wC[i] = *(const uint2*)&su[C3 + (tb + i) * 8 + ng * 2];
-    }
-    float yp[4];
-    #pragma unroll
-    for (int i = 0; i < 4; ++i) {
-      float dl = dodd ? hi16(wd[i]) : lo16(wd[i]);
-      float u = dl * (dodd ? hi16(wx[i]) : lo16(wx[i]));
-      float e0 = EXP2F(Av.x * dl), e1 = EXP2F(Av.y * dl);
-      float e2 = EXP2F(Av.z * dl), e3 = EXP2F(Av.w * dl);
-      h0 = fmaf(e0, h0, u * lo16(wB[i].x));
-      h1 = fmaf(e1, h1, u * hi16(wB[i].x));
-      h2 = fmaf(e2, h2, u * lo16(wB[i].y));
-      h3 = fmaf(e3, h3, u * hi16(wB[i].y));
-      float y = h0 * lo16(wC[i].x);
-      y = fmaf(h1, hi16(wC[i].x), y);
-      y = fmaf(h2, lo16(wC[i].y), y);
-      y = fmaf(h3, hi16(wC[i].y), y);
-      yp[i] = y;
-    }
-    #pragma unroll
-    for (int i = 0; i < 4; ++i) yp[i] += __shfl_xor(yp[i], 1);
-    #pragma unroll
-    for (int i = 0; i < 4; ++i) yp[i] += __shfl_xor(yp[i], 2);
-    float ysel = ng == 0 ? yp[0] : ng == 1 ? yp[1] : ng == 2 ? yp[2] : yp[3];
-    s[YOF + (tb + ng) * 17 + d] = ysel;
+    float4 Av = *(float4*)&s[SW_A + d * 16 + ng * 4];
+    float h0 = 0.f, h1 = 0.f, h2 = 0.f, h3 = 0.f, sd = 0.f;
+    for (int tile = 0; tile < 8; ++tile) {
+      int tb = t0 + tile * 4;
+      unsigned wd[4], wx[4]; uint2 wB[4];
+      #pragma unroll
+      for (int i = 0; i < 4; ++i) {
+        int base = REC + (tb + i) * RSTR;
+        wd[i] = su32[base + dh];
+        wx[i] = su32[base + 8 + dh];
+        wB[i] = *(const uint2*)&su32[base + 16 + ng * 2];
+      }
+      #pragma unroll
+      for (int i = 0; i < 4; ++i) {
+        float dl = dodd ? hi16(wd[i]) : lo16(wd[i]);
+        float u = dl * (dodd ? hi16(wx[i]) : lo16(wx[i]));
+        float e0 = EXP2F(Av.x * dl), e1 = EXP2F(Av.y * dl);
+        float e2 = EXP2F(Av.z * dl), e3 = EXP2F(Av.w * dl);
+        h0 = fmaf(e0, h0, u * lo16(wB[i].x));
+        h1 = fmaf(e1, h1, u * hi16(wB[i].x));
+        h2 = fmaf(e2, h2, u * lo16(wB[i].y));
+        h3 = fmaf(e3, h3, u * hi16(wB[i].y));
+        sd += dl;
+      }
+    }
+    su32[SCRH + w * 128 + d * 8 + ng * 2]     = pk(h0, h1);
+    su32[SCRH + w * 128 + d * 8 + ng * 2 + 1] = pk(h2, h3);
+    if (ng == 0) s[SCRS + w * 16 + d] = sd;
+  }
+  __syncthreads();
+  int dd = tid >> 3, pr = tid & 7;
+  float A0 = 0.f, A1 = 0.f;
+  if (tid < 128) {
+    A0 = s[SW_A + dd * 16 + pr * 2];
+    A1 = s[SW_A + dd * 16 + pr * 2 + 1];
+    float Sag = 0.f, hA0 = 0.f, hA1 = 0.f;
+    #pragma unroll
+    for (int w_ = 0; w_ < 4; ++w_) {
+      unsigned lw = su32[SCRH + w_ * 128 + dd * 8 + pr];
+      float sw = s[SCRS + w_ * 16 + dd];
+      float e0 = EXP2F(A0 * sw), e1 = EXP2F(A1 * sw);
+      hA0 = fmaf(e0, hA0, lo16(lw));
+      hA1 = fmaf(e1, hA1, hi16(lw));
+      Sag += sw;
+    }
+    __hip_atomic_store(&((unsigned*)p.agg)[cid * AGGW + 16 + dd * 8 + pr],
+                       pk(hA0, hA1), __ATOMIC_RELAXED, __HIP_MEMORY_SCOPE_AGENT);
+    if (pr == 0)
+      __hip_atomic_store(&p.agg[cid * AGGW + dd], Sag,
+                         __ATOMIC_RELAXED, __HIP_MEMORY_SCOPE_AGENT);
+  }
+  __threadfence();
+  __syncthreads();
+  if (tid == 0) atomicExch(&p.flags[cid], 1u);
+  for (int j = c0 + tid; j < cid; j += 256)
+    while (__hip_atomic_load(&p.flags[j], __ATOMIC_RELAXED,
+                             __HIP_MEMORY_SCOPE_AGENT) == 0u)
+      __builtin_amdgcn_s_sleep(8);
+  __syncthreads();
+  if (tid < 128) {
+    float hp0 = 0.f, hp1 = 0.f;
+    for (int j = c0; j < cid; ++j) {
+      float sv = __hip_atomic_load(&p.agg[j * AGGW + dd],
+                                   __ATOMIC_RELAXED, __HIP_MEMORY_SCOPE_AGENT);
+      unsigned hw = __hip_atomic_load(&((unsigned*)p.agg)[j * AGGW + 16 + dd * 8 + pr],
+                                      __ATOMIC_RELAXED, __HIP_MEMORY_SCOPE_AGENT);
+      float e0 = EXP2F(A0 * sv), e1 = EXP2F(A1 * sv);
+      hp0 = fmaf(e0, hp0, lo16(hw));
+      hp1 = fmaf(e1, hp1, hi16(hw));
+    }
+    #pragma unroll
+    for (int w_ = 0; w_ < 4; ++w_) {
+      unsigned lw = su32[SCRH + w_ * 128 + dd * 8 + pr];
+      float sw = s[SCRS + w_ * 16 + dd];
+      su32[SCRH + w_ * 128 + dd * 8 + pr] = pk(hp0, hp1);
+      float e0 = EXP2F(A0 * sw), e1 = EXP2F(A1 * sw);
+      hp0 = fmaf(e0, hp0, lo16(lw));
+      hp1 = fmaf(e1, hp1, hi16(lw));
+    }
+  }
+  __syncthreads();
+  {
+    float4 Av = *(float4*)&s[SW_A + d * 16 + ng * 4];
+    unsigned hw0 = su32[SCRH + w * 128 + d * 8 + ng * 2];
+    unsigned hw1 = su32[SCRH + w * 128 + d * 8 + ng * 2 + 1];
+    float h0 = lo16(hw0), h1 = hi16(hw0), h2 = lo16(hw1), h3 = hi16(hw1);
+    for (int tile = 0; tile < 8; ++tile) {
+      int tb = t0 + tile * 4;
+      unsigned wd[4], wx[4]; uint2 wB[4], wC[4];
+      #pragma unroll
+      for (int i = 0; i < 4; ++i) {
+        int base = REC + (tb + i) * RSTR;
+        wd[i] = su32[base + dh];
+        wx[i] = su32[base + 8 + dh];
+        wB[i] = *(const uint2*)&su32[base + 16 + ng * 2];
+        wC[i] = *(const uint2*)&su32[C3f + (tb + i) * 8 + ng * 2];
+      }
+      float yp[4];
+      #pragma unroll
+      for (int i = 0; i < 4; ++i) {
+        float dl = dodd ? hi16(wd[i]) : lo16(wd[i]);
+        float u = dl * (dodd ? hi16(wx[i]) : lo16(wx[i]));
+        float e0 = EXP2F(Av.x * dl), e1 = EXP2F(Av.y * dl);
+        float e2 = EXP2F(Av.z * dl), e3 = EXP2F(Av.w * dl);
+        h0 = fmaf(e0, h0, u * lo16(wB[i].x));
+        h1 = fmaf(e1, h1, u * hi16(wB[i].x));
+        h2 = fmaf(e2, h2, u * lo16(wB[i].y));
+        h3 = fmaf(e3, h3, u * hi16(wB[i].y));
+        float y = h0 * lo16(wC[i].x);
+        y = fmaf(h1, hi16(wC[i].x), y);
+        y = fmaf(h2, lo16(wC[i].y), y);
+        y = fmaf(h3, hi16(wC[i].y), y);
+        yp[i] = y;
+      }
+      #pragma unroll
+      for (int i = 0; i < 4; ++i) yp[i] += __shfl_xor(yp[i], 1);
+      #pragma unroll
+      for (int i = 0; i < 4; ++i) yp[i] += __shfl_xor(yp[i], 2);
+      float ysel = ng == 0 ? yp[0] : ng == 1 ? yp[1] : ng == 2 ? yp[2] : yp[3];
+      float yo = __shfl_xor(ysel, 4);
+      if (!(d & 1))
+        su32[C3f + (tb + ng) * 8 + (d >> 1)] = pk(ysel, yo);
+    }
   }
   __syncthreads();
   if (tok < Sa) {
-    const unsigned* xp = (const unsigned*)&s[X83 + tok * 4];
+    const unsigned* xp = &su32[X83f + tok * 4];
     float c8[8];
     #pragma unroll
     for (int q = 0; q < 4; ++q) { c8[2*q] = lo16(xp[q]); c8[2*q+1] = hi16(xp[q]); }
-    const unsigned* ru = (const unsigned*)&s[REC + tok * RSTR];
     float yv8[8];
     #pragma unroll
     for (int q = 0; q < 4; ++q) {
       unsigned wv = ru[8 + hf * 4 + q];
+      unsigned yw = su32[C3f + tok * 8 + hf * 4 + q];
       int d0 = ch0 + 2 * q;
       float4 w0a = *(const float4*)&s[SW_IN + (16 + d0) * 8];
       float4 w0b = *(const float4*)&s[SW_IN + (16 + d0) * 8 + 4];
@@ -639,8 +598,8 @@
       z1 = fmaf(w1a.y, c8[1], z1); z1 = fmaf(w1a.z, c8[2], z1); z1 = fmaf(w1a.w, c8[3], z1);
       z1 = fmaf(w1b.x, c8[4], z1); z1 = fmaf(w1b.y, c8[5], z1);
       z1 = fmaf(w1b.z, c8[6], z1); z1 = fmaf(w1b.w, c8[7], z1);
-      yv8[2*q]   = (s[YOF + tok * 17 + d0]     + lo16(wv) * s[SW_D + d0])     * siluf(z0);
-      yv8[2*q+1] = (s[YOF + tok * 17 + d0 + 1] + hi16(wv) * s[SW_D + d0 + 1]) * siluf(z1);
+      yv8[2*q]   = (lo16(yw) + lo16(wv) * s[SW_D + d0])     * siluf(z0);
+      yv8[2*q+1] = (hi16(yw) + hi16(wv) * s[SW_D + d0 + 1]) * siluf(z1);
     }
     float o[8];
     float sk = s[SW_SKIP];
@@ -720,10 +679,8 @@
   p.skip = (const float*)d_in[31];
   p.out = (float*)d_out;
   float* ws = (float*)d_ws;
-  p.hloc     = ws;
-  p.sumdelta = ws + (size_t)NSUB * 128;
-  p.grec     = ws + (size_t)NSUB * 128 + (size_t)NSUB * 16;
-  k_pass1<<<dim3(NCHUNK), dim3(256), 0, stream>>>(p);
-  k_pass2<<<dim3(512), dim3(256), 0, stream>>>(p);
-  k_pass3<<<dim3(NCHUNK + 8), dim3(256), 0, stream>>>(p);
-}
+  p.flags = (unsigned*)ws;
+  p.agg   = ws + 2048;
+  hipMemsetAsync(d_ws, 0, 2048 * sizeof(unsigned), stream);
+  k_fused<<<dim3(NCHUNK + 8), dim3(256), 0, stream>>>(p);
+}
```

Result: slower. 275.2 us (+141.6%).
